# Optimization experiments

Measured on AMD Instinct MI355X. Metric: run time of the kernel, lower is better.

## Reference

```python
import jax, jax.numpy as jnp
import numpy as np

NUM_EXPERTS = 8
HIDDEN = 2048
EXPERT_DIM = 4096
R = 64
LORA_ALPHA = 16
SCALING = LORA_ALPHA / R
TOKENS_PER_EXPERT = 1024


def setup_inputs() -> dict:
    key = jax.random.key(0)
    ks = jax.random.split(key, 7)
    s = lambda shape: 1.0 / np.sqrt(shape[-1])
    return {
        "hidden_states": jax.random.normal(ks[0], (NUM_EXPERTS * TOKENS_PER_EXPERT, HIDDEN), jnp.float32),
        "W_gu": jax.random.normal(ks[1], (2 * EXPERT_DIM, HIDDEN), jnp.float32) * s((HIDDEN,)),
        "A_gu": jax.random.normal(ks[2], (R, HIDDEN), jnp.float32) * s((HIDDEN,)),
        "B_gu": jax.random.normal(ks[3], (2 * EXPERT_DIM, R), jnp.float32) * 0.01,
        "W_d": jax.random.normal(ks[4], (HIDDEN, EXPERT_DIM), jnp.float32) * s((EXPERT_DIM,)),
        "A_d": jax.random.normal(ks[5], (R, EXPERT_DIM), jnp.float32) * s((EXPERT_DIM,)),
        "B_d": jax.random.normal(ks[6], (HIDDEN, R), jnp.float32) * 0.01,
    }


def _lora_linear(x, W, A, B):
    # y = x @ W^T + scaling * (x @ A^T) @ B^T   (nn.Linear convention, no dropout)
    return x @ W.T + (x @ A.T) @ B.T * SCALING


def reference(hidden_states, W_gu, A_gu, B_gu, W_d, A_d, B_d):
    # (E, N, H)
    x = hidden_states.reshape(NUM_EXPERTS, -1, HIDDEN)
    gate_up = _lora_linear(x, W_gu, A_gu, B_gu)          # (E, N, 2*D)
    gate, up = jnp.split(gate_up, 2, axis=-1)             # each (E, N, D)
    h = up * jax.nn.silu(gate)                            # SwiGLU
    out = _lora_linear(h, W_d, A_d, B_d)                  # (E, N, H)
    return out.reshape(-1, HIDDEN)
```

## Files before the change

### kernel.cpp

```cpp
#include <hip/hip_runtime.h>
#include <stdint.h>

typedef __bf16 bf16_t;
typedef __bf16 bf16x8 __attribute__((ext_vector_type(8)));
typedef __bf16 bf16x4 __attribute__((ext_vector_type(4)));
typedef float f32x4 __attribute__((ext_vector_type(4)));

#define GLOAD16(gp, lp)                                                        \
    __builtin_amdgcn_global_load_lds(                                          \
        (const __attribute__((address_space(1))) void*)(gp),                   \
        (__attribute__((address_space(3))) void*)(lp), 16, 0, 0)


__global__ __launch_bounds__(256) void cvt_all_kernel(
    const float* __restrict__ x, const float* __restrict__ Wgu,
    const float* __restrict__ Bgu, const float* __restrict__ Wd,
    const float* __restrict__ Bd, const float* __restrict__ Agu,
    const float* __restrict__ Ad, bf16_t* __restrict__ X1,
    bf16_t* __restrict__ W1, bf16_t* __restrict__ W2,
    bf16_t* __restrict__ Abf, bf16_t* __restrict__ Adbf) {
    int b = blockIdx.x;
    const float* src;
    bf16_t* dst;
    int cshift, cmask, ldd, coff, lb;
    if (b < 16384) {
        src = x; dst = X1; cshift = 11; cmask = 2047; ldd = 2112; coff = 0; lb = b;
    } else if (b < 32768) {
        src = Wgu; dst = W1; cshift = 11; cmask = 2047; ldd = 2112; coff = 0; lb = b - 16384;
    } else if (b < 33280) {
        src = Bgu; dst = W1; cshift = 6; cmask = 63; ldd = 2112; coff = 2048; lb = b - 32768;
    } else if (b < 41472) {
        src = Wd; dst = W2; cshift = 12; cmask = 4095; ldd = 4160; coff = 0; lb = b - 33280;
    } else if (b < 41600) {
        src = Bd; dst = W2; cshift = 6; cmask = 63; ldd = 4160; coff = 4096; lb = b - 41472;
    } else if (b < 41728) {
        src = Agu; dst = Abf; cshift = 11; cmask = 2047; ldd = 2048; coff = 0; lb = b - 41600;
    } else {
        src = Ad; dst = Adbf; cshift = 12; cmask = 4095; ldd = 4096; coff = 0; lb = b - 41728;
    }
    int idx = (lb * 256 + threadIdx.x) << 2;
    int r = idx >> cshift;
    int c = idx & cmask;
    float4 v = *(const float4*)(src + idx);
    bf16x4 o = {(bf16_t)v.x, (bf16_t)v.y, (bf16_t)v.z, (bf16_t)v.w};
    *(bf16x4*)(dst + (size_t)r * ldd + coff + c) = o;
}

__global__ __launch_bounds__(256) void lora_kernel(const bf16_t* __restrict__ A,
                                                   int lda,
                                                   const bf16_t* __restrict__ Bw,
                                                   int K, bf16_t* __restrict__ dst,
                                                   int ldd, int coff) {
    __shared__ __align__(16) bf16_t As[64 * 64];
    __shared__ __align__(16) bf16_t Bs[64 * 64];
    const int t = threadIdx.x;
    const int m0 = blockIdx.x * 64;
    const int lane = t & 63, w = t >> 6;
    const int ln15 = lane & 15, q = lane >> 4;

    const int lrow = t >> 3;
    const int lchunk = (t & 7) ^ (lrow & 7);
    const bf16_t* gaL = A + (size_t)(m0 + lrow) * lda + lchunk * 8;
    const bf16_t* gbL = Bw + (size_t)lrow * K + lchunk * 8;
    bf16_t* lA = As + t * 8;
    bf16_t* lB = Bs + t * 8;

    const f32x4 z = {0.f, 0.f, 0.f, 0.f};
    f32x4 acc[4];
#pragma unroll
    for (int j = 0; j < 4; ++j) acc[j] = z;

    int aoffs[2], boffs[2][4];
#pragma unroll
    for (int s = 0; s < 2; ++s) {
        int rowa = w * 16 + ln15;
        aoffs[s] = rowa * 64 + (((q + 4 * s) ^ (rowa & 7)) << 3);
#pragma unroll
        for (int j = 0; j < 4; ++j) {
            int rowb = j * 16 + ln15;
            boffs[s][j] = rowb * 64 + (((q + 4 * s) ^ (rowb & 7)) << 3);
        }
    }

    for (int kt = 0; kt < K; kt += 64) {
        GLOAD16(gaL, lA);
        GLOAD16(gaL + (size_t)32 * lda, lA + 32 * 64);
        GLOAD16(gbL, lB);
        GLOAD16(gbL + (size_t)32 * K, lB + 32 * 64);
        __syncthreads();
#pragma unroll
        for (int s = 0; s < 2; ++s) {
            bf16x8 av = *(const bf16x8*)(As + aoffs[s]);
#pragma unroll
            for (int j = 0; j < 4; ++j) {
                bf16x8 bv = *(const bf16x8*)(Bs + boffs[s][j]);
                acc[j] = __builtin_amdgcn_mfma_f32_16x16x32_bf16(av, bv, acc[j], 0, 0, 0);
            }
        }
        __syncthreads();
        gaL += 64;
        gbL += 64;
    }

#pragma unroll
    for (int j = 0; j < 4; ++j)
#pragma unroll
        for (int rg = 0; rg < 4; ++rg) {
            int m = m0 + w * 16 + q * 4 + rg;
            dst[(size_t)m * ldd + coff + j * 16 + ln15] = (bf16_t)(acc[j][rg] * 0.25f);
        }
}

__global__ __launch_bounds__(256, 4) void gemm1_kernel(const bf16_t* __restrict__ X,
                                                       const bf16_t* __restrict__ Wc,
                                                       bf16_t* __restrict__ X2) {
    constexpr int LDA = 2112, LDW = 2112, LDX2 = 4160, K = 2112;
    __shared__ __align__(16) bf16_t As[128 * 64];
    __shared__ __align__(16) bf16_t Bs[128 * 64];
    const int t = threadIdx.x;
    const int n0 = blockIdx.x * 64;
    const int m0 = blockIdx.y * 128;
    const int lane = t & 63, w = t >> 6, wr = w >> 1, wc = w & 1;
    const int ln15 = lane & 15, q = lane >> 4;

    const int lrow = t >> 3;
    const int lchunk = (t & 7) ^ (lrow & 7);
    const bf16_t* gaL = X + (size_t)(m0 + lrow) * LDA + lchunk * 8;
    const bf16_t* gbgL = Wc + (size_t)(n0 + lrow) * LDW + lchunk * 8;
    const bf16_t* gbuL = Wc + (size_t)(4096 + n0 + lrow) * LDW + lchunk * 8;
    bf16_t* lA = As + t * 8;
    bf16_t* lB = Bs + t * 8;

    const f32x4 z = {0.f, 0.f, 0.f, 0.f};
    f32x4 accg[4][2], accu[4][2];
#pragma unroll
    for (int i = 0; i < 4; ++i)
#pragma unroll
        for (int j = 0; j < 2; ++j) {
            accg[i][j] = z;
            accu[i][j] = z;
        }

    int aoffs[2][4], bgoffs[2][2];
#pragma unroll
    for (int s = 0; s < 2; ++s) {
#pragma unroll
        for (int i = 0; i < 4; ++i) {
            int row = wr * 64 + i * 16 + ln15;
            aoffs[s][i] = row * 64 + (((q + 4 * s) ^ (row & 7)) << 3);
        }
#pragma unroll
        for (int j = 0; j < 2; ++j) {
            int row = wc * 32 + j * 16 + ln15;
            bgoffs[s][j] = row * 64 + (((q + 4 * s) ^ (row & 7)) << 3);
        }
    }

    for (int kt = 0; kt < K; kt += 64) {
        GLOAD16(gaL, lA);
        GLOAD16(gaL + (size_t)32 * LDA, lA + 32 * 64);
        GLOAD16(gaL + (size_t)64 * LDA, lA + 64 * 64);
        GLOAD16(gaL + (size_t)96 * LDA, lA + 96 * 64);
        GLOAD16(gbgL, lB);
        GLOAD16(gbgL + (size_t)32 * LDW, lB + 32 * 64);
        GLOAD16(gbuL, lB + 64 * 64);
        GLOAD16(gbuL + (size_t)32 * LDW, lB + 96 * 64);
        __syncthreads();
#pragma unroll
        for (int s = 0; s < 2; ++s) {
            bf16x8 av[4], bg[2], bu[2];
#pragma unroll
            for (int i = 0; i < 4; ++i) av[i] = *(const bf16x8*)(As + aoffs[s][i]);
#pragma unroll
            for (int j = 0; j < 2; ++j) {
                bg[j] = *(const bf16x8*)(Bs + bgoffs[s][j]);
                bu[j] = *(const bf16x8*)(Bs + bgoffs[s][j] + 64 * 64);
            }
#pragma unroll
            for (int i = 0; i < 4; ++i)
#pragma unroll
                for (int j = 0; j < 2; ++j) {
                    accg[i][j] = __builtin_amdgcn_mfma_f32_16x16x32_bf16(av[i], bg[j], accg[i][j], 0, 0, 0);
                    accu[i][j] = __builtin_amdgcn_mfma_f32_16x16x32_bf16(av[i], bu[j], accu[i][j], 0, 0, 0);
                }
        }
        __syncthreads();
        gaL += 64;
        gbgL += 64;
        gbuL += 64;
    }

#pragma unroll
    for (int i = 0; i < 4; ++i)
#pragma unroll
        for (int j = 0; j < 2; ++j)
#pragma unroll
            for (int rg = 0; rg < 4; ++rg) {
                int m = m0 + wr * 64 + i * 16 + q * 4 + rg;
                int d = n0 + wc * 32 + j * 16 + ln15;
                float g = accg[i][j][rg];
                float u = accu[i][j][rg];
                float h = u * g / (1.f + __expf(-g));
                X2[(size_t)m * LDX2 + d] = (bf16_t)h;
            }
}

__global__ __launch_bounds__(256, 4) void gemm2_kernel(const bf16_t* __restrict__ X2,
                                                       const bf16_t* __restrict__ Wdc,
                                                       float* __restrict__ out) {
    constexpr int LDA = 4160, LDB = 4160, K = 4160, LDO = 2048;
    __shared__ __align__(16) bf16_t As[128 * 64];
    __shared__ __align__(16) bf16_t Bs[128 * 64];
    const int t = threadIdx.x;
    const int n0 = blockIdx.x * 128;
    const int m0 = blockIdx.y * 128;
    const int lane = t & 63, w = t >> 6, wr = w >> 1, wc = w & 1;
    const int ln15 = lane & 15, q = lane >> 4;

    const int lrow = t >> 3;
    const int lchunk = (t & 7) ^ (lrow & 7);
    const bf16_t* gaL = X2 + (size_t)(m0 + lrow) * LDA + lchunk * 8;
    const bf16_t* gbL = Wdc + (size_t)(n0 + lrow) * LDB + lchunk * 8;
    bf16_t* lA = As + t * 8;
    bf16_t* lB = Bs + t * 8;

    const f32x4 z = {0.f, 0.f, 0.f, 0.f};
    f32x4 acc[4][4];
#pragma unroll
    for (int i = 0; i < 4; ++i)
#pragma unroll
        for (int j = 0; j < 4; ++j) acc[i][j] = z;

    int aoffs[2][4], boffs[2][4];
#pragma unroll
    for (int s = 0; s < 2; ++s)
#pragma unroll
        for (int i = 0; i < 4; ++i) {
            int rowa = wr * 64 + i * 16 + ln15;
            int rowb = wc * 64 + i * 16 + ln15;
            aoffs[s][i] = rowa * 64 + (((q + 4 * s) ^ (rowa & 7)) << 3);
            boffs[s][i] = rowb * 64 + (((q + 4 * s) ^ (rowb & 7)) << 3);
        }

    for (int kt = 0; kt < K; kt += 64) {
        GLOAD16(gaL, lA);
        GLOAD16(gaL + (size_t)32 * LDA, lA + 32 * 64);
        GLOAD16(gaL + (size_t)64 * LDA, lA + 64 * 64);
        GLOAD16(gaL + (size_t)96 * LDA, lA + 96 * 64);
        GLOAD16(gbL, lB);
        GLOAD16(gbL + (size_t)32 * LDB, lB + 32 * 64);
        GLOAD16(gbL + (size_t)64 * LDB, lB + 64 * 64);
        GLOAD16(gbL + (size_t)96 * LDB, lB + 96 * 64);
        __syncthreads();
#pragma unroll
        for (int s = 0; s < 2; ++s) {
            bf16x8 av[4], bv[4];
#pragma unroll
            for (int i = 0; i < 4; ++i) {
                av[i] = *(const bf16x8*)(As + aoffs[s][i]);
                bv[i] = *(const bf16x8*)(Bs + boffs[s][i]);
            }
#pragma unroll
            for (int i = 0; i < 4; ++i)
#pragma unroll
                for (int j = 0; j < 4; ++j)
                    acc[i][j] = __builtin_amdgcn_mfma_f32_16x16x32_bf16(av[i], bv[j], acc[i][j], 0, 0, 0);
        }
        __syncthreads();
        gaL += 64;
        gbL += 64;
    }

#pragma unroll
    for (int i = 0; i < 4; ++i)
#pragma unroll
        for (int j = 0; j < 4; ++j)
#pragma unroll
            for (int rg = 0; rg < 4; ++rg) {
                int m = m0 + wr * 64 + i * 16 + q * 4 + rg;
                int n = n0 + wc * 64 + j * 16 + ln15;
                out[(size_t)m * LDO + n] = acc[i][j][rg];
            }
}

extern "C" void kernel_launch(void* const* d_in, const int* in_sizes, int n_in,
                              void* d_out, int out_size, void* d_ws, size_t ws_size,
                              hipStream_t stream) {
    const float* x = (const float*)d_in[0];
    const float* Wgu = (const float*)d_in[1];
    const float* Agu = (const float*)d_in[2];
    const float* Bgu = (const float*)d_in[3];
    const float* Wd = (const float*)d_in[4];
    const float* Ad = (const float*)d_in[5];
    const float* Bd = (const float*)d_in[6];
    float* out = (float*)d_out;

    char* ws = (char*)d_ws;
    bf16_t* X1 = (bf16_t*)(ws);
    bf16_t* W1 = (bf16_t*)(ws + 34603008);
    bf16_t* X2 = (bf16_t*)(ws + 69206016);
    bf16_t* W2 = (bf16_t*)(ws + 137363456);
    bf16_t* Abf = (bf16_t*)(ws + 154402816);
    bf16_t* Adbf = (bf16_t*)(ws + 154664960);

    cvt_all_kernel<<<41984, 256, 0, stream>>>(x, Wgu, Bgu, Wd, Bd, Agu, Ad,
                                              X1, W1, W2, Abf, Adbf);

    lora_kernel<<<128, 256, 0, stream>>>(X1, 2112, Abf, 2048, X1, 2112, 2048);
    gemm1_kernel<<<dim3(64, 64), 256, 0, stream>>>(X1, W1, X2);
    lora_kernel<<<128, 256, 0, stream>>>(X2, 4160, Adbf, 4096, X2, 4160, 4096);
    gemm2_kernel<<<dim3(16, 64), 256, 0, stream>>>(X2, W2, out);
}
```

Baseline: 638.9 us.

## Replace GEMM kernels with 256x256 8-wave double-buffered ping-pong pipeline

Both main GEMMs move to a shared 8-wave (512-thread) core that computes 256x256 tiles with double-buffered LDS. Global-to-LDS loads are split into four phases interleaved with MFMA clusters, with raw s_barrier, waitcnt and setprio used to overlap memory with compute. For gemm1 the gate and up columns land in different waves, so the SwiGLU epilogue exchanges them through LDS. The larger tiles cut global traffic per FLOP, at the cost of a 128KB LDS footprint, limited occupancy and fragile hand-written synchronisation.

After: 627.8 us. Within noise of the previous version (-1.7%).

```diff
diff --git a/kernel.cpp b/kernel.cpp
--- a/kernel.cpp
+++ b/kernel.cpp
@@ -10,6 +10,23 @@
     __builtin_amdgcn_global_load_lds(                                          \
         (const __attribute__((address_space(1))) void*)(gp),                   \
         (__attribute__((address_space(3))) void*)(lp), 16, 0, 0)
+
+#define MFMA16(a, b, c) __builtin_amdgcn_mfma_f32_16x16x32_bf16(a, b, c, 0, 0, 0)
+
+#define PH_PRE()                                                               \
+    do {                                                                       \
+        __builtin_amdgcn_sched_barrier(0);                                     \
+        asm volatile("s_barrier" ::: "memory");                                \
+        asm volatile("s_waitcnt lgkmcnt(0)" ::: "memory");                     \
+        __builtin_amdgcn_sched_barrier(0);                                     \
+        __builtin_amdgcn_s_setprio(1);                                         \
+    } while (0)
+#define PH_POST()                                                              \
+    do {                                                                       \
+        __builtin_amdgcn_s_setprio(0);                                         \
+        __builtin_amdgcn_sched_barrier(0);                                     \
+        asm volatile("s_barrier" ::: "memory");                                \
+    } while (0)
 
 
 __global__ __launch_bounds__(256) void cvt_all_kernel(
@@ -94,7 +111,7 @@
 #pragma unroll
             for (int j = 0; j < 4; ++j) {
                 bf16x8 bv = *(const bf16x8*)(Bs + boffs[s][j]);
-                acc[j] = __builtin_amdgcn_mfma_f32_16x16x32_bf16(av, bv, acc[j], 0, 0, 0);
+                acc[j] = MFMA16(av, bv, acc[j]);
             }
         }
         __syncthreads();
@@ -111,175 +128,233 @@
         }
 }
 
-__global__ __launch_bounds__(256, 4) void gemm1_kernel(const bf16_t* __restrict__ X,
-                                                       const bf16_t* __restrict__ Wc,
-                                                       bf16_t* __restrict__ X2) {
-    constexpr int LDA = 2112, LDW = 2112, LDX2 = 4160, K = 2112;
-    __shared__ __align__(16) bf16_t As[128 * 64];
-    __shared__ __align__(16) bf16_t Bs[128 * 64];
+template <int LDA_, int LDB_, int NT_>
+__device__ __forceinline__ void gemm8p_core(const bf16_t* __restrict__ gA,
+                                            const bf16_t* __restrict__ gB0,
+                                            const bf16_t* __restrict__ gB2,
+                                            bf16_t* smem, const int t,
+                                            const int offA0, const int offA1,
+                                            const int offB0, const int offB1,
+                                            f32x4 (&acc)[8][4]) {
+    auto stgA0 = [&](int kt, bf16_t* d) {
+        GLOAD16(gA + kt, d + t * 8);
+        GLOAD16(gA + (size_t)128 * LDA_ + kt, d + 128 * 64 + t * 8);
+    };
+    auto stgA1 = [&](int kt, bf16_t* d) {
+        GLOAD16(gA + (size_t)64 * LDA_ + kt, d + 64 * 64 + t * 8);
+        GLOAD16(gA + (size_t)192 * LDA_ + kt, d + 192 * 64 + t * 8);
+    };
+    auto stgBlo = [&](int kt, bf16_t* d) {
+        GLOAD16(gB0 + kt, d + t * 8);
+        GLOAD16(gB0 + (size_t)64 * LDB_ + kt, d + 64 * 64 + t * 8);
+    };
+    auto stgBhi = [&](int kt, bf16_t* d) {
+        GLOAD16(gB2 + kt, d + 128 * 64 + t * 8);
+        GLOAD16(gB2 + (size_t)64 * LDB_ + kt, d + 192 * 64 + t * 8);
+    };
+
+    bf16_t* const As0 = smem;
+    bf16_t* const As1 = smem + 16384;
+    bf16_t* const Bs0 = smem + 32768;
+    bf16_t* const Bs1 = smem + 49152;
+
+    stgA0(0, As0);
+    stgA1(0, As0);
+    stgBlo(0, Bs0);
+    stgBhi(0, Bs0);
+    stgA0(64, As1);
+    stgBlo(64, Bs1);
+    stgBhi(64, Bs1);
+    asm volatile("s_waitcnt vmcnt(6)" ::: "memory");
+    asm volatile("s_barrier" ::: "memory");
+
+    bf16x8 av[4][2], b0[2][2], b1[2][2];
+    for (int g = 0; g < NT_; ++g) {
+        const int bs = (g & 1) << 14;
+        bf16_t* const Asc = smem + bs;
+        bf16_t* const Bsc = smem + 32768 + bs;
+        bf16_t* const Asn = smem + (bs ^ 16384);
+        const int k1 = (g + 1) << 6, k2 = (g + 2) << 6;
+
+#pragma unroll
+        for (int m = 0; m < 4; ++m) {
+            av[m][0] = *(const bf16x8*)(Asc + offA0 + m * 1024);
+            av[m][1] = *(const bf16x8*)(Asc + offA1 + m * 1024);
+        }
+#pragma unroll
+        for (int n = 0; n < 2; ++n) {
+            b0[n][0] = *(const bf16x8*)(Bsc + offB0 + n * 1024);
+            b0[n][1] = *(const bf16x8*)(Bsc + offB1 + n * 1024);
+        }
+        if (g + 1 < NT_) stgA1(k1, Asn);
+        PH_PRE();
+#pragma unroll
+        for (int m = 0; m < 4; ++m)
+#pragma unroll
+            for (int n = 0; n < 2; ++n) {
+                acc[m][n] = MFMA16(av[m][0], b0[n][0], acc[m][n]);
+                acc[m][n] = MFMA16(av[m][1], b0[n][1], acc[m][n]);
+            }
+        PH_POST();
+
+#pragma unroll
+        for (int n = 0; n < 2; ++n) {
+            b1[n][0] = *(const bf16x8*)(Bsc + offB0 + (2 + n) * 1024);
+            b1[n][1] = *(const bf16x8*)(Bsc + offB1 + (2 + n) * 1024);
+        }
+        if (g + 2 < NT_) stgA0(k2, Asc);
+        PH_PRE();
+#pragma unroll
+        for (int m = 0; m < 4; ++m)
+#pragma unroll
+            for (int n = 0; n < 2; ++n) {
+                acc[m][2 + n] = MFMA16(av[m][0], b1[n][0], acc[m][2 + n]);
+                acc[m][2 + n] = MFMA16(av[m][1], b1[n][1], acc[m][2 + n]);
+            }
+        PH_POST();
+
+#pragma unroll
+        for (int m = 0; m < 4; ++m) {
+            av[m][0] = *(const bf16x8*)(Asc + offA0 + (4 + m) * 1024);
+            av[m][1] = *(const bf16x8*)(Asc + offA1 + (4 + m) * 1024);
+        }
+        if (g + 2 < NT_) stgBlo(k2, Bsc);
+        PH_PRE();
+#pragma unroll
+        for (int m = 0; m < 4; ++m)
+#pragma unroll
+            for (int n = 0; n < 2; ++n) {
+                acc[4 + m][2 + n] = MFMA16(av[m][0], b1[n][0], acc[4 + m][2 + n]);
+                acc[4 + m][2 + n] = MFMA16(av[m][1], b1[n][1], acc[4 + m][2 + n]);
+            }
+        PH_POST();
+
+        if (g + 2 < NT_) stgBhi(k2, Bsc);
+        PH_PRE();
+#pragma unroll
+        for (int m = 0; m < 4; ++m)
+#pragma unroll
+            for (int n = 0; n < 2; ++n) {
+                acc[4 + m][n] = MFMA16(av[m][0], b0[n][0], acc[4 + m][n]);
+                acc[4 + m][n] = MFMA16(av[m][1], b0[n][1], acc[4 + m][n]);
+            }
+        __builtin_amdgcn_s_setprio(0);
+        __builtin_amdgcn_sched_barrier(0);
+        if (g + 2 < NT_)
+            asm volatile("s_waitcnt vmcnt(6)" ::: "memory");
+        else
+            asm volatile("s_waitcnt vmcnt(0)" ::: "memory");
+        asm volatile("s_barrier" ::: "memory");
+    }
+}
+
+__global__ __launch_bounds__(512, 2) void gemm1_8p_kernel(
+    const bf16_t* __restrict__ X, const bf16_t* __restrict__ Wc,
+    bf16_t* __restrict__ X2) {
+    __shared__ __align__(16) bf16_t smem[65536];
     const int t = threadIdx.x;
-    const int n0 = blockIdx.x * 64;
-    const int m0 = blockIdx.y * 128;
-    const int lane = t & 63, w = t >> 6, wr = w >> 1, wc = w & 1;
+    const int lane = t & 63, wid = t >> 6;
+    const int wr = wid >> 2, wc = wid & 3;
     const int ln15 = lane & 15, q = lane >> 4;
-
-    const int lrow = t >> 3;
-    const int lchunk = (t & 7) ^ (lrow & 7);
-    const bf16_t* gaL = X + (size_t)(m0 + lrow) * LDA + lchunk * 8;
-    const bf16_t* gbgL = Wc + (size_t)(n0 + lrow) * LDW + lchunk * 8;
-    const bf16_t* gbuL = Wc + (size_t)(4096 + n0 + lrow) * LDW + lchunk * 8;
-    bf16_t* lA = As + t * 8;
-    bf16_t* lB = Bs + t * 8;
-
+    const int n0 = blockIdx.x * 128;
+    const int m0 = blockIdx.y * 256;
+
+    const int sw = ln15 & 7;
+    const int offA0 = (wr * 128 + ln15) * 64 + ((q ^ sw) << 3);
+    const int offA1 = (wr * 128 + ln15) * 64 + (((q + 4) ^ sw) << 3);
+    const int offB0 = (wc * 64 + ln15) * 64 + ((q ^ sw) << 3);
+    const int offB1 = (wc * 64 + ln15) * 64 + (((q + 4) ^ sw) << 3);
+
+    const int rr = t >> 3;
+    const int lch = (t & 7) ^ (rr & 7);
+    const bf16_t* gA = X + (size_t)(m0 + rr) * 2112 + lch * 8;
+    const bf16_t* gB0 = Wc + (size_t)(n0 + rr) * 2112 + lch * 8;
+    const bf16_t* gB2 = Wc + (size_t)(4096 + n0 + rr) * 2112 + lch * 8;
+
+    f32x4 acc[8][4];
     const f32x4 z = {0.f, 0.f, 0.f, 0.f};
-    f32x4 accg[4][2], accu[4][2];
-#pragma unroll
-    for (int i = 0; i < 4; ++i)
-#pragma unroll
-        for (int j = 0; j < 2; ++j) {
-            accg[i][j] = z;
-            accu[i][j] = z;
-        }
-
-    int aoffs[2][4], bgoffs[2][2];
-#pragma unroll
-    for (int s = 0; s < 2; ++s) {
-#pragma unroll
-        for (int i = 0; i < 4; ++i) {
-            int row = wr * 64 + i * 16 + ln15;
-            aoffs[s][i] = row * 64 + (((q + 4 * s) ^ (row & 7)) << 3);
-        }
-#pragma unroll
-        for (int j = 0; j < 2; ++j) {
-            int row = wc * 32 + j * 16 + ln15;
-            bgoffs[s][j] = row * 64 + (((q + 4 * s) ^ (row & 7)) << 3);
-        }
-    }
-
-    for (int kt = 0; kt < K; kt += 64) {
-        GLOAD16(gaL, lA);
-        GLOAD16(gaL + (size_t)32 * LDA, lA + 32 * 64);
-        GLOAD16(gaL + (size_t)64 * LDA, lA + 64 * 64);
-        GLOAD16(gaL + (size_t)96 * LDA, lA + 96 * 64);
-        GLOAD16(gbgL, lB);
-        GLOAD16(gbgL + (size_t)32 * LDW, lB + 32 * 64);
-        GLOAD16(gbuL, lB + 64 * 64);
-        GLOAD16(gbuL + (size_t)32 * LDW, lB + 96 * 64);
-        __syncthreads();
-#pragma unroll
-        for (int s = 0; s < 2; ++s) {
-            bf16x8 av[4], bg[2], bu[2];
-#pragma unroll
-            for (int i = 0; i < 4; ++i) av[i] = *(const bf16x8*)(As + aoffs[s][i]);
-#pragma unroll
-            for (int j = 0; j < 2; ++j) {
-                bg[j] = *(const bf16x8*)(Bs + bgoffs[s][j]);
-                bu[j] = *(const bf16x8*)(Bs + bgoffs[s][j] + 64 * 64);
-            }
-#pragma unroll
-            for (int i = 0; i < 4; ++i)
-#pragma unroll
-                for (int j = 0; j < 2; ++j) {
-                    accg[i][j] = __builtin_amdgcn_mfma_f32_16x16x32_bf16(av[i], bg[j], accg[i][j], 0, 0, 0);
-                    accu[i][j] = __builtin_amdgcn_mfma_f32_16x16x32_bf16(av[i], bu[j], accu[i][j], 0, 0, 0);
+#pragma unroll
+    for (int i = 0; i < 8; ++i)
+#pragma unroll
+        for (int j = 0; j < 4; ++j) acc[i][j] = z;
+
+    gemm8p_core<2112, 2112, 33>(gA, gB0, gB2, smem, t, offA0, offA1, offB0,
+                                offB1, acc);
+
+    __syncthreads();
+    float* fs = (float*)smem;
+    if (wc >= 2) {
+#pragma unroll
+        for (int mi = 0; mi < 8; ++mi)
+#pragma unroll
+            for (int nj = 0; nj < 4; ++nj)
+#pragma unroll
+                for (int rg = 0; rg < 4; ++rg) {
+                    int row = wr * 128 + mi * 16 + q * 4 + rg;
+                    int col = (wc - 2) * 64 + nj * 16 + ln15;
+                    fs[row * 128 + col] = acc[mi][nj][rg];
                 }
-        }
-        __syncthreads();
-        gaL += 64;
-        gbgL += 64;
-        gbuL += 64;
-    }
-
-#pragma unroll
-    for (int i = 0; i < 4; ++i)
-#pragma unroll
-        for (int j = 0; j < 2; ++j)
+    }
+    __syncthreads();
+    if (wc < 2) {
+#pragma unroll
+        for (int mi = 0; mi < 8; ++mi)
+#pragma unroll
+            for (int nj = 0; nj < 4; ++nj)
+#pragma unroll
+                for (int rg = 0; rg < 4; ++rg) {
+                    int row = wr * 128 + mi * 16 + q * 4 + rg;
+                    int col = wc * 64 + nj * 16 + ln15;
+                    float gv = acc[mi][nj][rg];
+                    float uv = fs[row * 128 + col];
+                    float h = uv * gv / (1.f + __expf(-gv));
+                    X2[(size_t)(m0 + row) * 4160 + (n0 + col)] = (bf16_t)h;
+                }
+    }
+}
+
+__global__ __launch_bounds__(512, 2) void gemm2_8p_kernel(
+    const bf16_t* __restrict__ X2, const bf16_t* __restrict__ Wdc,
+    float* __restrict__ out) {
+    __shared__ __align__(16) bf16_t smem[65536];
+    const int t = threadIdx.x;
+    const int lane = t & 63, wid = t >> 6;
+    const int wr = wid >> 2, wc = wid & 3;
+    const int ln15 = lane & 15, q = lane >> 4;
+    const int n0 = blockIdx.x * 256;
+    const int m0 = blockIdx.y * 256;
+
+    const int sw = ln15 & 7;
+    const int offA0 = (wr * 128 + ln15) * 64 + ((q ^ sw) << 3);
+    const int offA1 = (wr * 128 + ln15) * 64 + (((q + 4) ^ sw) << 3);
+    const int offB0 = (wc * 64 + ln15) * 64 + ((q ^ sw) << 3);
+    const int offB1 = (wc * 64 + ln15) * 64 + (((q + 4) ^ sw) << 3);
+
+    const int rr = t >> 3;
+    const int lch = (t & 7) ^ (rr & 7);
+    const bf16_t* gA = X2 + (size_t)(m0 + rr) * 4160 + lch * 8;
+    const bf16_t* gB0 = Wdc + (size_t)(n0 + rr) * 4160 + lch * 8;
+    const bf16_t* gB2 = Wdc + (size_t)(n0 + 128 + rr) * 4160 + lch * 8;
+
+    f32x4 acc[8][4];
+    const f32x4 z = {0.f, 0.f, 0.f, 0.f};
+#pragma unroll
+    for (int i = 0; i < 8; ++i)
+#pragma unroll
+        for (int j = 0; j < 4; ++j) acc[i][j] = z;
+
+    gemm8p_core<4160, 4160, 65>(gA, gB0, gB2, smem, t, offA0, offA1, offB0,
+                                offB1, acc);
+
+#pragma unroll
+    for (int mi = 0; mi < 8; ++mi)
+#pragma unroll
+        for (int nj = 0; nj < 4; ++nj)
 #pragma unroll
             for (int rg = 0; rg < 4; ++rg) {
-                int m = m0 + wr * 64 + i * 16 + q * 4 + rg;
-                int d = n0 + wc * 32 + j * 16 + ln15;
-                float g = accg[i][j][rg];
-                float u = accu[i][j][rg];
-                float h = u * g / (1.f + __expf(-g));
-                X2[(size_t)m * LDX2 + d] = (bf16_t)h;
-            }
-}
-
-__global__ __launch_bounds__(256, 4) void gemm2_kernel(const bf16_t* __restrict__ X2,
-                                                       const bf16_t* __restrict__ Wdc,
-                                                       float* __restrict__ out) {
-    constexpr int LDA = 4160, LDB = 4160, K = 4160, LDO = 2048;
-    __shared__ __align__(16) bf16_t As[128 * 64];
-    __shared__ __align__(16) bf16_t Bs[128 * 64];
-    const int t = threadIdx.x;
-    const int n0 = blockIdx.x * 128;
-    const int m0 = blockIdx.y * 128;
-    const int lane = t & 63, w = t >> 6, wr = w >> 1, wc = w & 1;
-    const int ln15 = lane & 15, q = lane >> 4;
-
-    const int lrow = t >> 3;
-    const int lchunk = (t & 7) ^ (lrow & 7);
-    const bf16_t* gaL = X2 + (size_t)(m0 + lrow) * LDA + lchunk * 8;
-    const bf16_t* gbL = Wdc + (size_t)(n0 + lrow) * LDB + lchunk * 8;
-    bf16_t* lA = As + t * 8;
-    bf16_t* lB = Bs + t * 8;
-
-    const f32x4 z = {0.f, 0.f, 0.f, 0.f};
-    f32x4 acc[4][4];
-#pragma unroll
-    for (int i = 0; i < 4; ++i)
-#pragma unroll
-        for (int j = 0; j < 4; ++j) acc[i][j] = z;
-
-    int aoffs[2][4], boffs[2][4];
-#pragma unroll
-    for (int s = 0; s < 2; ++s)
-#pragma unroll
-        for (int i = 0; i < 4; ++i) {
-            int rowa = wr * 64 + i * 16 + ln15;
-            int rowb = wc * 64 + i * 16 + ln15;
-            aoffs[s][i] = rowa * 64 + (((q + 4 * s) ^ (rowa & 7)) << 3);
-            boffs[s][i] = rowb * 64 + (((q + 4 * s) ^ (rowb & 7)) << 3);
-        }
-
-    for (int kt = 0; kt < K; kt += 64) {
-        GLOAD16(gaL, lA);
-        GLOAD16(gaL + (size_t)32 * LDA, lA + 32 * 64);
-        GLOAD16(gaL + (size_t)64 * LDA, lA + 64 * 64);
-        GLOAD16(gaL + (size_t)96 * LDA, lA + 96 * 64);
-        GLOAD16(gbL, lB);
-        GLOAD16(gbL + (size_t)32 * LDB, lB + 32 * 64);
-        GLOAD16(gbL + (size_t)64 * LDB, lB + 64 * 64);
-        GLOAD16(gbL + (size_t)96 * LDB, lB + 96 * 64);
-        __syncthreads();
-#pragma unroll
-        for (int s = 0; s < 2; ++s) {
-            bf16x8 av[4], bv[4];
-#pragma unroll
-            for (int i = 0; i < 4; ++i) {
-                av[i] = *(const bf16x8*)(As + aoffs[s][i]);
-                bv[i] = *(const bf16x8*)(Bs + boffs[s][i]);
-            }
-#pragma unroll
-            for (int i = 0; i < 4; ++i)
-#pragma unroll
-                for (int j = 0; j < 4; ++j)
-                    acc[i][j] = __builtin_amdgcn_mfma_f32_16x16x32_bf16(av[i], bv[j], acc[i][j], 0, 0, 0);
-        }
-        __syncthreads();
-        gaL += 64;
-        gbL += 64;
-    }
-
-#pragma unroll
-    for (int i = 0; i < 4; ++i)
-#pragma unroll
-        for (int j = 0; j < 4; ++j)
-#pragma unroll
-            for (int rg = 0; rg < 4; ++rg) {
-                int m = m0 + wr * 64 + i * 16 + q * 4 + rg;
-                int n = n0 + wc * 64 + j * 16 + ln15;
-                out[(size_t)m * LDO + n] = acc[i][j][rg];
+                int row = wr * 128 + mi * 16 + q * 4 + rg;
+                int col = wc * 64 + nj * 16 + ln15;
+                out[(size_t)(m0 + row) * 2048 + (n0 + col)] = acc[mi][nj][rg];
             }
 }
 
@@ -307,7 +382,7 @@
                                               X1, W1, W2, Abf, Adbf);
 
     lora_kernel<<<128, 256, 0, stream>>>(X1, 2112, Abf, 2048, X1, 2112, 2048);
-    gemm1_kernel<<<dim3(64, 64), 256, 0, stream>>>(X1, W1, X2);
+    gemm1_8p_kernel<<<dim3(32, 32), 512, 0, stream>>>(X1, W1, X2);
     lora_kernel<<<128, 256, 0, stream>>>(X2, 4160, Adbf, 4096, X2, 4160, 4096);
-    gemm2_kernel<<<dim3(16, 64), 256, 0, stream>>>(X2, W2, out);
-}
+    gemm2_8p_kernel<<<dim3(8, 32), 512, 0, stream>>>(X2, W2, out);
+}
```

## Enlarge GEMM M-tiles to 256 rows and double-buffer LoRA kernel loads

Applied to the files above, without the earlier changes.

The two main GEMMs now compute 256-row M tiles per block, so each wave holds an 8x4 accumulator grid and reuses each loaded B fragment across twice as many MFMAs. The grids are halved to match and occupancy is lowered to 2 blocks per SM. This cuts global and LDS traffic per FLOP but raises register pressure and reduces the number of resident blocks. Separately, the LoRA down-projection kernel gets a two-stage LDS double buffer with explicit vmcnt waits and barriers, so the next K tile loads while the current one is computed.

After: 615.1 us. -3.7%, faster.

```diff
diff --git a/kernel.cpp b/kernel.cpp
--- a/kernel.cpp
+++ b/kernel.cpp
@@ -10,6 +10,12 @@
     __builtin_amdgcn_global_load_lds(                                          \
         (const __attribute__((address_space(1))) void*)(gp),                   \
         (__attribute__((address_space(3))) void*)(lp), 16, 0, 0)
+
+#define MFMA16(a, b, c) __builtin_amdgcn_mfma_f32_16x16x32_bf16(a, b, c, 0, 0, 0)
+
+#define BAR() asm volatile("s_barrier" ::: "memory")
+#define LGKM0() asm volatile("s_waitcnt lgkmcnt(0)" ::: "memory")
+#define VMW(n) asm volatile("s_waitcnt vmcnt(" #n ")" ::: "memory")
 
 
 __global__ __launch_bounds__(256) void cvt_all_kernel(
@@ -51,8 +57,8 @@
                                                    const bf16_t* __restrict__ Bw,
                                                    int K, bf16_t* __restrict__ dst,
                                                    int ldd, int coff) {
-    __shared__ __align__(16) bf16_t As[64 * 64];
-    __shared__ __align__(16) bf16_t Bs[64 * 64];
+    __shared__ __align__(16) bf16_t As[2 * 64 * 64];
+    __shared__ __align__(16) bf16_t Bs[2 * 64 * 64];
     const int t = threadIdx.x;
     const int m0 = blockIdx.x * 64;
     const int lane = t & 63, w = t >> 6;
@@ -62,8 +68,6 @@
     const int lchunk = (t & 7) ^ (lrow & 7);
     const bf16_t* gaL = A + (size_t)(m0 + lrow) * lda + lchunk * 8;
     const bf16_t* gbL = Bw + (size_t)lrow * K + lchunk * 8;
-    bf16_t* lA = As + t * 8;
-    bf16_t* lB = Bs + t * 8;
 
     const f32x4 z = {0.f, 0.f, 0.f, 0.f};
     f32x4 acc[4];
@@ -82,24 +86,35 @@
         }
     }
 
-    for (int kt = 0; kt < K; kt += 64) {
-        GLOAD16(gaL, lA);
-        GLOAD16(gaL + (size_t)32 * lda, lA + 32 * 64);
-        GLOAD16(gbL, lB);
-        GLOAD16(gbL + (size_t)32 * K, lB + 32 * 64);
-        __syncthreads();
+    auto stage = [&](int kt, int bo) {
+        GLOAD16(gaL + kt, As + bo + t * 8);
+        GLOAD16(gaL + kt + (size_t)32 * lda, As + bo + 2048 + t * 8);
+        GLOAD16(gbL + kt, Bs + bo + t * 8);
+        GLOAD16(gbL + kt + (size_t)32 * K, Bs + bo + 2048 + t * 8);
+    };
+
+    const int NT = K >> 6;
+    stage(0, 0);
+    for (int g = 0; g < NT; ++g) {
+        const bool more = (g + 1) < NT;
+        if (more) stage((g + 1) << 6, ((g + 1) & 1) * 4096);
+        if (more)
+            VMW(4);
+        else
+            VMW(0);
+        BAR();
+        const int bo = (g & 1) * 4096;
 #pragma unroll
         for (int s = 0; s < 2; ++s) {
-            bf16x8 av = *(const bf16x8*)(As + aoffs[s]);
+            bf16x8 av = *(const bf16x8*)(As + bo + aoffs[s]);
 #pragma unroll
             for (int j = 0; j < 4; ++j) {
-                bf16x8 bv = *(const bf16x8*)(Bs + boffs[s][j]);
-                acc[j] = __builtin_amdgcn_mfma_f32_16x16x32_bf16(av, bv, acc[j], 0, 0, 0);
-            }
-        }
-        __syncthreads();
-        gaL += 64;
-        gbL += 64;
+                bf16x8 bv = *(const bf16x8*)(Bs + bo + boffs[s][j]);
+                acc[j] = MFMA16(av, bv, acc[j]);
+            }
+        }
+        LGKM0();
+        BAR();
     }
 
 #pragma unroll
@@ -111,15 +126,15 @@
         }
 }
 
-__global__ __launch_bounds__(256, 4) void gemm1_kernel(const bf16_t* __restrict__ X,
+__global__ __launch_bounds__(256, 2) void gemm1_kernel(const bf16_t* __restrict__ X,
                                                        const bf16_t* __restrict__ Wc,
                                                        bf16_t* __restrict__ X2) {
     constexpr int LDA = 2112, LDW = 2112, LDX2 = 4160, K = 2112;
-    __shared__ __align__(16) bf16_t As[128 * 64];
+    __shared__ __align__(16) bf16_t As[256 * 64];
     __shared__ __align__(16) bf16_t Bs[128 * 64];
     const int t = threadIdx.x;
     const int n0 = blockIdx.x * 64;
-    const int m0 = blockIdx.y * 128;
+    const int m0 = blockIdx.y * 256;
     const int lane = t & 63, w = t >> 6, wr = w >> 1, wc = w & 1;
     const int ln15 = lane & 15, q = lane >> 4;
 
@@ -132,35 +147,29 @@
     bf16_t* lB = Bs + t * 8;
 
     const f32x4 z = {0.f, 0.f, 0.f, 0.f};
-    f32x4 accg[4][2], accu[4][2];
-#pragma unroll
-    for (int i = 0; i < 4; ++i)
-#pragma unroll
-        for (int j = 0; j < 2; ++j) {
-            accg[i][j] = z;
-            accu[i][j] = z;
-        }
-
-    int aoffs[2][4], bgoffs[2][2];
-#pragma unroll
-    for (int s = 0; s < 2; ++s) {
-#pragma unroll
-        for (int i = 0; i < 4; ++i) {
-            int row = wr * 64 + i * 16 + ln15;
-            aoffs[s][i] = row * 64 + (((q + 4 * s) ^ (row & 7)) << 3);
-        }
-#pragma unroll
-        for (int j = 0; j < 2; ++j) {
-            int row = wc * 32 + j * 16 + ln15;
-            bgoffs[s][j] = row * 64 + (((q + 4 * s) ^ (row & 7)) << 3);
-        }
-    }
+    f32x4 acc[8][4];
+#pragma unroll
+    for (int i = 0; i < 8; ++i)
+#pragma unroll
+        for (int j = 0; j < 4; ++j) acc[i][j] = z;
+
+    const int sw7 = ln15 & 7;
+    const int arow = wr * 128 + ln15;
+    const int aoff0 = arow * 64 + ((q ^ sw7) << 3);
+    const int aoff1 = arow * 64 + (((q + 4) ^ sw7) << 3);
+    const int brow = wc * 32 + ln15;
+    const int boff0 = brow * 64 + ((q ^ sw7) << 3);
+    const int boff1 = brow * 64 + (((q + 4) ^ sw7) << 3);
 
     for (int kt = 0; kt < K; kt += 64) {
         GLOAD16(gaL, lA);
         GLOAD16(gaL + (size_t)32 * LDA, lA + 32 * 64);
         GLOAD16(gaL + (size_t)64 * LDA, lA + 64 * 64);
         GLOAD16(gaL + (size_t)96 * LDA, lA + 96 * 64);
+        GLOAD16(gaL + (size_t)128 * LDA, lA + 128 * 64);
+        GLOAD16(gaL + (size_t)160 * LDA, lA + 160 * 64);
+        GLOAD16(gaL + (size_t)192 * LDA, lA + 192 * 64);
+        GLOAD16(gaL + (size_t)224 * LDA, lA + 224 * 64);
         GLOAD16(gbgL, lB);
         GLOAD16(gbgL + (size_t)32 * LDW, lB + 32 * 64);
         GLOAD16(gbuL, lB + 64 * 64);
@@ -168,21 +177,25 @@
         __syncthreads();
 #pragma unroll
         for (int s = 0; s < 2; ++s) {
-            bf16x8 av[4], bg[2], bu[2];
-#pragma unroll
-            for (int i = 0; i < 4; ++i) av[i] = *(const bf16x8*)(As + aoffs[s][i]);
-#pragma unroll
-            for (int j = 0; j < 2; ++j) {
-                bg[j] = *(const bf16x8*)(Bs + bgoffs[s][j]);
-                bu[j] = *(const bf16x8*)(Bs + bgoffs[s][j] + 64 * 64);
-            }
-#pragma unroll
-            for (int i = 0; i < 4; ++i)
-#pragma unroll
-                for (int j = 0; j < 2; ++j) {
-                    accg[i][j] = __builtin_amdgcn_mfma_f32_16x16x32_bf16(av[i], bg[j], accg[i][j], 0, 0, 0);
-                    accu[i][j] = __builtin_amdgcn_mfma_f32_16x16x32_bf16(av[i], bu[j], accu[i][j], 0, 0, 0);
-                }
+            const int ao = s ? aoff1 : aoff0;
+            const int bo = s ? boff1 : boff0;
+            bf16x8 bv[4];
+            bv[0] = *(const bf16x8*)(Bs + bo);
+            bv[1] = *(const bf16x8*)(Bs + bo + 1024);
+            bv[2] = *(const bf16x8*)(Bs + bo + 64 * 64);
+            bv[3] = *(const bf16x8*)(Bs + bo + 64 * 64 + 1024);
+#pragma unroll
+            for (int g2 = 0; g2 < 2; ++g2) {
+                bf16x8 av[4];
+#pragma unroll
+                for (int i = 0; i < 4; ++i)
+                    av[i] = *(const bf16x8*)(As + ao + (g2 * 4 + i) * 1024);
+#pragma unroll
+                for (int i = 0; i < 4; ++i)
+#pragma unroll
+                    for (int j = 0; j < 4; ++j)
+                        acc[g2 * 4 + i][j] = MFMA16(av[i], bv[j], acc[g2 * 4 + i][j]);
+            }
         }
         __syncthreads();
         gaL += 64;
@@ -191,29 +204,29 @@
     }
 
 #pragma unroll
-    for (int i = 0; i < 4; ++i)
-#pragma unroll
-        for (int j = 0; j < 2; ++j)
+    for (int mi = 0; mi < 8; ++mi)
+#pragma unroll
+        for (int nj = 0; nj < 2; ++nj)
 #pragma unroll
             for (int rg = 0; rg < 4; ++rg) {
-                int m = m0 + wr * 64 + i * 16 + q * 4 + rg;
-                int d = n0 + wc * 32 + j * 16 + ln15;
-                float g = accg[i][j][rg];
-                float u = accu[i][j][rg];
+                int m = m0 + wr * 128 + mi * 16 + q * 4 + rg;
+                int d = n0 + wc * 32 + nj * 16 + ln15;
+                float g = acc[mi][nj][rg];
+                float u = acc[mi][nj + 2][rg];
                 float h = u * g / (1.f + __expf(-g));
                 X2[(size_t)m * LDX2 + d] = (bf16_t)h;
             }
 }
 
-__global__ __launch_bounds__(256, 4) void gemm2_kernel(const bf16_t* __restrict__ X2,
+__global__ __launch_bounds__(256, 2) void gemm2_kernel(const bf16_t* __restrict__ X2,
                                                        const bf16_t* __restrict__ Wdc,
                                                        float* __restrict__ out) {
     constexpr int LDA = 4160, LDB = 4160, K = 4160, LDO = 2048;
-    __shared__ __align__(16) bf16_t As[128 * 64];
+    __shared__ __align__(16) bf16_t As[256 * 64];
     __shared__ __align__(16) bf16_t Bs[128 * 64];
     const int t = threadIdx.x;
     const int n0 = blockIdx.x * 128;
-    const int m0 = blockIdx.y * 128;
+    const int m0 = blockIdx.y * 256;
     const int lane = t & 63, w = t >> 6, wr = w >> 1, wc = w & 1;
     const int ln15 = lane & 15, q = lane >> 4;
 
@@ -225,28 +238,29 @@
     bf16_t* lB = Bs + t * 8;
 
     const f32x4 z = {0.f, 0.f, 0.f, 0.f};
-    f32x4 acc[4][4];
-#pragma unroll
-    for (int i = 0; i < 4; ++i)
+    f32x4 acc[8][4];
+#pragma unroll
+    for (int i = 0; i < 8; ++i)
 #pragma unroll
         for (int j = 0; j < 4; ++j) acc[i][j] = z;
 
-    int aoffs[2][4], boffs[2][4];
-#pragma unroll
-    for (int s = 0; s < 2; ++s)
-#pragma unroll
-        for (int i = 0; i < 4; ++i) {
-            int rowa = wr * 64 + i * 16 + ln15;
-            int rowb = wc * 64 + i * 16 + ln15;
-            aoffs[s][i] = rowa * 64 + (((q + 4 * s) ^ (rowa & 7)) << 3);
-            boffs[s][i] = rowb * 64 + (((q + 4 * s) ^ (rowb & 7)) << 3);
-        }
+    const int sw7 = ln15 & 7;
+    const int arow = wr * 128 + ln15;
+    const int aoff0 = arow * 64 + ((q ^ sw7) << 3);
+    const int aoff1 = arow * 64 + (((q + 4) ^ sw7) << 3);
+    const int brow = wc * 64 + ln15;
+    const int boff0 = brow * 64 + ((q ^ sw7) << 3);
+    const int boff1 = brow * 64 + (((q + 4) ^ sw7) << 3);
 
     for (int kt = 0; kt < K; kt += 64) {
         GLOAD16(gaL, lA);
         GLOAD16(gaL + (size_t)32 * LDA, lA + 32 * 64);
         GLOAD16(gaL + (size_t)64 * LDA, lA + 64 * 64);
         GLOAD16(gaL + (size_t)96 * LDA, lA + 96 * 64);
+        GLOAD16(gaL + (size_t)128 * LDA, lA + 128 * 64);
+        GLOAD16(gaL + (size_t)160 * LDA, lA + 160 * 64);
+        GLOAD16(gaL + (size_t)192 * LDA, lA + 192 * 64);
+        GLOAD16(gaL + (size_t)224 * LDA, lA + 224 * 64);
         GLOAD16(gbL, lB);
         GLOAD16(gbL + (size_t)32 * LDB, lB + 32 * 64);
         GLOAD16(gbL + (size_t)64 * LDB, lB + 64 * 64);
@@ -254,17 +268,24 @@
         __syncthreads();
 #pragma unroll
         for (int s = 0; s < 2; ++s) {
-            bf16x8 av[4], bv[4];
-#pragma unroll
-            for (int i = 0; i < 4; ++i) {
-                av[i] = *(const bf16x8*)(As + aoffs[s][i]);
-                bv[i] = *(const bf16x8*)(Bs + boffs[s][i]);
-            }
-#pragma unroll
-            for (int i = 0; i < 4; ++i)
-#pragma unroll
-                for (int j = 0; j < 4; ++j)
-                    acc[i][j] = __builtin_amdgcn_mfma_f32_16x16x32_bf16(av[i], bv[j], acc[i][j], 0, 0, 0);
+            const int ao = s ? aoff1 : aoff0;
+            const int bo = s ? boff1 : boff0;
+            bf16x8 bv[4];
+#pragma unroll
+            for (int j = 0; j < 4; ++j)
+                bv[j] = *(const bf16x8*)(Bs + bo + j * 1024);
+#pragma unroll
+            for (int g2 = 0; g2 < 2; ++g2) {
+                bf16x8 av[4];
+#pragma unroll
+                for (int i = 0; i < 4; ++i)
+                    av[i] = *(const bf16x8*)(As + ao + (g2 * 4 + i) * 1024);
+#pragma unroll
+                for (int i = 0; i < 4; ++i)
+#pragma unroll
+                    for (int j = 0; j < 4; ++j)
+                        acc[g2 * 4 + i][j] = MFMA16(av[i], bv[j], acc[g2 * 4 + i][j]);
+            }
         }
         __syncthreads();
         gaL += 64;
@@ -272,14 +293,14 @@
     }
 
 #pragma unroll
-    for (int i = 0; i < 4; ++i)
-#pragma unroll
-        for (int j = 0; j < 4; ++j)
+    for (int mi = 0; mi < 8; ++mi)
+#pragma unroll
+        for (int nj = 0; nj < 4; ++nj)
 #pragma unroll
             for (int rg = 0; rg < 4; ++rg) {
-                int m = m0 + wr * 64 + i * 16 + q * 4 + rg;
-                int n = n0 + wc * 64 + j * 16 + ln15;
-                out[(size_t)m * LDO + n] = acc[i][j][rg];
+                int m = m0 + wr * 128 + mi * 16 + q * 4 + rg;
+                int n = n0 + wc * 64 + nj * 16 + ln15;
+                out[(size_t)m * LDO + n] = acc[mi][nj][rg];
             }
 }
 
@@ -307,7 +328,7 @@
                                               X1, W1, W2, Abf, Adbf);
 
     lora_kernel<<<128, 256, 0, stream>>>(X1, 2112, Abf, 2048, X1, 2112, 2048);
-    gemm1_kernel<<<dim3(64, 64), 256, 0, stream>>>(X1, W1, X2);
+    gemm1_kernel<<<dim3(64, 32), 256, 0, stream>>>(X1, W1, X2);
     lora_kernel<<<128, 256, 0, stream>>>(X2, 4160, Adbf, 4096, X2, 4160, 4096);
-    gemm2_kernel<<<dim3(16, 64), 256, 0, stream>>>(X2, W2, out);
-}
+    gemm2_kernel<<<dim3(16, 32), 256, 0, stream>>>(X2, W2, out);
+}
```
